# Kernel tuning notes

Measured on AMD Instinct MI355X. Metric: run time of the kernel, lower is better.

## Reference

```python
import jax, jax.numpy as jnp
import numpy as np

N, F, H, E = 100000, 128, 128, 3200000
EPS = 1e-5


def setup_inputs() -> dict:
    key = jax.random.key(0)
    ks = jax.random.split(key, 16)
    g = lambda k, shape, fan_in: jax.random.normal(k, shape, jnp.float32) / np.sqrt(fan_in)
    inp = {
        'x': jax.random.normal(ks[0], (N, F), jnp.float32),
        'edge_index': jax.random.randint(ks[1], (2, E), 0, N, jnp.int64),
        # SAGEConv params: lin_l (aggregated-neighbor path, has bias), lin_r (root path, no bias)
        'W1l': g(ks[2], (F, H), F), 'b1': jnp.zeros((H,), jnp.float32), 'W1r': g(ks[3], (F, H), F),
        'W2l': g(ks[4], (H, H), H), 'b2': jnp.zeros((H,), jnp.float32), 'W2r': g(ks[5], (H, H), H),
        'W3l': g(ks[6], (H, H), H), 'b3': jnp.zeros((H,), jnp.float32), 'W3r': g(ks[7], (H, H), H),
        'W4l': g(ks[8], (H, 1), H), 'b4': jnp.zeros((1,), jnp.float32), 'W4r': g(ks[9], (H, 1), H),
        # BatchNorm affine params
        'g1': jnp.ones((H,), jnp.float32), 'be1': jnp.zeros((H,), jnp.float32),
        'g2': jnp.ones((H,), jnp.float32), 'be2': jnp.zeros((H,), jnp.float32),
        'g3': jnp.ones((H,), jnp.float32), 'be3': jnp.zeros((H,), jnp.float32),
        # shared residual linear
        'Wlin': g(ks[10], (H, H), H), 'blin': jnp.zeros((H,), jnp.float32),
    }
    return inp


def _sage(x, src, dst, Wl, b, Wr):
    # mean aggregation of source features at destination nodes
    n = x.shape[0]
    s = jax.ops.segment_sum(x[src], dst, num_segments=n)          # [N, d]
    cnt = jax.ops.segment_sum(jnp.ones_like(dst, x.dtype), dst, num_segments=n)
    agg = s / jnp.maximum(cnt, 1.0)[:, None]
    return agg @ Wl + b + x @ Wr


def _bn(x, gamma, beta):
    # training-mode batch norm over node dim (biased variance, as torch)
    mu = x.mean(0)
    var = jnp.mean((x - mu) ** 2, axis=0)
    return gamma * (x - mu) * jax.lax.rsqrt(var + EPS) + beta


def reference(x, edge_index, W1l, b1, W1r, W2l, b2, W2r, W3l, b3, W3r,
              W4l, b4, W4r, g1, be1, g2, be2, g3, be3, Wlin, blin):
    src, dst = edge_index[0], edge_index[1]
    # dropout is identity (eval-mode reference)
    x1 = jax.nn.elu(_bn(_sage(x, src, dst, W1l, b1, W1r), g1, be1))
    x2 = jax.nn.elu(_bn(_sage(x1, src, dst, W2l, b2, W2r), g2, be2))
    x2 = x2 + x1 @ Wlin + blin
    x3 = jax.nn.elu(_bn(_sage(x2, src, dst, W3l, b3, W3r), g3, be3))
    x3 = x3 + x2 @ Wlin + blin
    x4 = _sage(x3, src, dst, W4l, b4, W4r)  # [N, 1]
    return jnp.squeeze(x4, -1)
```

## Files before the change

kernel.cpp:

```cpp
#include <hip/hip_runtime.h>
#include <hip/hip_bf16.h>
#include <math.h>

#define BN_EPS 1e-5f

typedef __attribute__((ext_vector_type(8))) short bf16x8;
typedef __attribute__((ext_vector_type(4))) float f32x4;
typedef unsigned int uint32;

__device__ __forceinline__ unsigned bf16rne(float f) {
  unsigned u = __float_as_uint(f);
  unsigned r = u + 0x7fffu + ((u >> 16) & 1u);
  return r >> 16;
}
__device__ __forceinline__ float bf2f_lo(uint32 u) { return __uint_as_float(u << 16); }
__device__ __forceinline__ float bf2f_hi(uint32 u) { return __uint_as_float(u & 0xffff0000u); }
__device__ __forceinline__ uint32 packbf2(float a, float b) {
  return bf16rne(a) | (bf16rne(b) << 16);
}

__device__ __forceinline__ int edge_at(const int* __restrict__ ei, long long idx, int is64) {
  return is64 ? ei[2 * idx] : ei[idx];
}

__global__ void init_kernel(const int* __restrict__ ei, long long E, int* __restrict__ flag,
                            int* __restrict__ cnt, float* __restrict__ bnsum, int N) {
  if (blockIdx.x == 0) {
    __shared__ int found;
    int t = threadIdx.x;
    if (t == 0) found = 0;
    __syncthreads();
    long long npairs = E < 1024 ? E : 1024;
    for (long long p = t; p < npairs; p += blockDim.x)
      if (ei[2 * p + 1] != 0) found = 1;
    __syncthreads();
    if (t == 0) *flag = found ? 0 : 1;
    return;
  }
  long long i = (blockIdx.x - 1) * (long long)blockDim.x + threadIdx.x;
  if (i < N) cnt[i] = 0;
  else if (i < (long long)N + 64 * 256) bnsum[i - N] = 0.f;
}

__launch_bounds__(256)
__global__ void build_kernel(const int* __restrict__ ei, long long E,
                             const int* __restrict__ flag,
                             int* __restrict__ r, int* __restrict__ cnt,
                             const float* __restrict__ x, uint32* __restrict__ xb,
                             long long nf4,
                             const float* __restrict__ Wa, const float* __restrict__ Wb,
                             const float* __restrict__ Wc, const float* __restrict__ Wd,
                             const float* __restrict__ We, const float* __restrict__ Wf,
                             const float* __restrict__ Wg, ushort* __restrict__ Wp,
                             long long K3) {
  long long b = blockIdx.x;
  if (b >= K3) {
    int rb = (int)(b - K3);
    int wi = rb >> 3;
    const float* W = wi == 0 ? Wa : wi == 1 ? Wb : wi == 2 ? Wc : wi == 3 ? Wd
                   : wi == 4 ? We : wi == 5 ? Wf : Wg;
    ushort* dst = Wp + (size_t)wi * 16384;
    int s = (rb & 7) * 256 + threadIdx.x;
    int nt = s >> 8, rem = s & 255, ks = rem >> 6, lane = rem & 63;
    int q = lane >> 4, l16 = lane & 15;
    int kbase = ks * 32 + q * 8, c = nt * 16 + l16;
    uint32 o[4];
#pragma unroll
    for (int jp = 0; jp < 4; ++jp) {
      float fa = W[(size_t)(kbase + 2 * jp) * 128 + c];
      float fb = W[(size_t)(kbase + 2 * jp + 1) * 128 + c];
      o[jp] = packbf2(fa, fb);
    }
    ((uint4*)dst)[s] = make_uint4(o[0], o[1], o[2], o[3]);
    return;
  }
  int role = (int)(b % 3);
  long long id = b / 3;
  if (role == 0) {
    long long g = id * 256 + threadIdx.x;
    long long e0 = 2 * g;
    if (e0 >= E) return;
    int is64 = *flag;
    bool h1 = (e0 + 1 < E);
    int d0, d1 = 0;
    if (is64 && !(E & 1)) {
      int4 dv = ((const int4*)(ei + 2 * E))[g];
      d0 = dv.x; d1 = dv.z;
    } else {
      d0 = edge_at(ei, E + e0, is64);
      if (h1) d1 = edge_at(ei, E + e0 + 1, is64);
    }
    int r0 = atomicAdd(&cnt[d0], 1);
    if (h1) {
      int r1 = atomicAdd(&cnt[d1], 1);
      ((int2*)r)[g] = make_int2(r0, r1);
    } else {
      r[e0] = r0;
    }
  } else {
    long long i = (id * 2 + (role - 1)) * 256 + threadIdx.x;
    if (i < nf4) {
      float4 f = ((const float4*)x)[i];
      uint2 o;
      o.x = packbf2(f.x, f.y);
      o.y = packbf2(f.z, f.w);
      ((uint2*)xb)[i] = o;
    }
  }
}

__global__ void partial_kernel(const int* __restrict__ cnt, int* __restrict__ bsum, int M) {
  __shared__ int s[256];
  int b = blockIdx.x, t = threadIdx.x;
  int base = b * 2048 + t * 8;
  int sum = 0;
#pragma unroll
  for (int i = 0; i < 8; ++i) {
    int idx = base + i;
    if (idx < M) sum += cnt[idx];
  }
  s[t] = sum;
  __syncthreads();
  for (int d = 128; d > 0; d >>= 1) {
    if (t < d) s[t] += s[t + d];
    __syncthreads();
  }
  if (t == 0) bsum[b] = s[0];
}

__global__ void scanb_kernel(int* __restrict__ bsum, int nb) {
  __shared__ int s[512];
  int t = threadIdx.x;
  int v = (t < nb) ? bsum[t] : 0;
  s[t] = v;
  __syncthreads();
  for (int d = 1; d < 512; d <<= 1) {
    int u = (t >= d) ? s[t - d] : 0;
    __syncthreads();
    s[t] += u;
    __syncthreads();
  }
  if (t < nb) bsum[t] = s[t] - v;
}

__global__ void offsets_kernel(const int* __restrict__ cnt, const int* __restrict__ bsum,
                               int* __restrict__ off, int M, long long Etot) {
  __shared__ int s[256];
  int b = blockIdx.x, t = threadIdx.x;
  int base = b * 2048 + t * 8;
  int v[8];
  int sum = 0;
#pragma unroll
  for (int i = 0; i < 8; ++i) {
    int idx = base + i;
    v[i] = (idx < M) ? cnt[idx] : 0;
    sum += v[i];
  }
  s[t] = sum;
  __syncthreads();
  for (int d = 1; d < 256; d <<= 1) {
    int u = (t >= d) ? s[t - d] : 0;
    __syncthreads();
    s[t] += u;
    __syncthreads();
  }
  int run = bsum[b] + s[t] - sum;
#pragma unroll
  for (int i = 0; i < 8; ++i) {
    int idx = base + i;
    if (idx < M) {
      off[idx] = run;
      run += v[i];
    }
  }
  if (b == 0 && t == 0) off[M] = (int)Etot;
}

__global__ void pos_scatter_kernel(const int* __restrict__ ei, long long E,
                                   const int* __restrict__ flag, const int* __restrict__ r,
                                   const int* __restrict__ off, uint32* __restrict__ ppk,
                                   int* __restrict__ esrc) {
  long long g = blockIdx.x * (long long)blockDim.x + threadIdx.x;
  long long e0 = 2 * g;
  if (e0 >= E) return;
  int is64 = *flag;
  bool h1 = (e0 + 1 < E);
  int d0, d1 = 0;
  if (is64 && !(E & 1)) {
    int4 dv = ((const int4*)(ei + 2 * E))[g];
    d0 = dv.x; d1 = dv.z;
  } else {
    d0 = edge_at(ei, E + e0, is64);
    if (h1) d1 = edge_at(ei, E + e0 + 1, is64);
  }
  int r0, r1 = 0;
  if (h1) { int2 rv = ((const int2*)r)[g]; r0 = rv.x; r1 = rv.y; }
  else r0 = r[e0];
  uint32 p0 = (uint32)(off[d0] + r0);
  uint32 reg0 = (uint32)d0 >> 15;
  ppk[e0] = p0 | (reg0 << 28);
  if (reg0 == 0) esrc[p0] = edge_at(ei, e0, is64);
  if (h1) {
    uint32 p1 = (uint32)(off[d1] + r1);
    uint32 reg1 = (uint32)d1 >> 15;
    ppk[e0 + 1] = p1 | (reg1 << 28);
    if (reg1 == 0) esrc[p1] = edge_at(ei, e0 + 1, is64);
  }
}

__global__ void scatter_det_kernel(const int* __restrict__ ei, long long E,
                                   const int* __restrict__ flag,
                                   const uint32* __restrict__ ppk, uint32 p,
                                   int* __restrict__ esrc) {
  long long e = blockIdx.x * (long long)blockDim.x + threadIdx.x;
  if (e >= E) return;
  uint32 v = ppk[e];
  if ((v >> 28) == p) esrc[v & 0x0FFFFFFFu] = edge_at(ei, e, *flag);
}

__global__ void aggregate_bf16_kernel(const uint32* __restrict__ X, const int* __restrict__ off,
                                      const int* __restrict__ esrc, uint32* __restrict__ out,
                                      int N) {
  int gw = (int)((blockIdx.x * (long long)blockDim.x + threadIdx.x) >> 6);
  int lane = threadIdx.x & 63;
  if (gw >= N) return;
  int b = off[gw], e = off[gw + 1];
  int sub = lane & 15, grp = lane >> 4;
  const uint4* X4 = (const uint4*)X;
  float acc[8];
#pragma unroll
  for (int j = 0; j < 8; ++j) acc[j] = 0.f;
  for (int i = b; i < e; i += 16) {
    uint4 v[4];
#pragma unroll
    for (int u = 0; u < 4; ++u) {
      int ii = i + u * 4 + grp;
      v[u] = make_uint4(0, 0, 0, 0);
      if (ii < e) { int s = esrc[ii]; v[u] = X4[(size_t)s * 16 + sub]; }
    }
#pragma unroll
    for (int u = 0; u < 4; ++u) {
      acc[0] += bf2f_lo(v[u].x); acc[1] += bf2f_hi(v[u].x);
      acc[2] += bf2f_lo(v[u].y); acc[3] += bf2f_hi(v[u].y);
      acc[4] += bf2f_lo(v[u].z); acc[5] += bf2f_hi(v[u].z);
      acc[6] += bf2f_lo(v[u].w); acc[7] += bf2f_hi(v[u].w);
    }
  }
#pragma unroll
  for (int j = 0; j < 8; ++j) {
    acc[j] += __shfl_xor(acc[j], 16, 64);
    acc[j] += __shfl_xor(acc[j], 32, 64);
  }
  if (grp == 0) {
    float inv = 1.0f / fmaxf((float)(e - b), 1.0f);
    uint4 o;
    o.x = packbf2(acc[0] * inv, acc[1] * inv);
    o.y = packbf2(acc[2] * inv, acc[3] * inv);
    o.z = packbf2(acc[4] * inv, acc[5] * inv);
    o.w = packbf2(acc[6] * inv, acc[7] * inv);
    ((uint4*)out)[(size_t)gw * 16 + sub] = o;
  }
}

__launch_bounds__(256)
__global__ void gemm_mfma_kernel(const ushort* __restrict__ A1, const ushort* __restrict__ W1p,
                                 const ushort* __restrict__ A2, const ushort* __restrict__ W2p,
                                 const ushort* __restrict__ W3p,
                                 const float* __restrict__ bias, const float* __restrict__ rbias,
                                 ushort* __restrict__ Y, ushort* __restrict__ R,
                                 float* __restrict__ bnsum, int N) {
  __shared__ float sred[16][128];
  int t = threadIdx.x;
  int w = t >> 6, lane = t & 63;
  int quad = lane >> 4, l16 = lane & 15;
  int row0 = blockIdx.x * 64 + w * 16;

  f32x4 accY[8], accR[8];
#pragma unroll
  for (int nt = 0; nt < 8; ++nt) {
    accY[nt][0] = accY[nt][1] = accY[nt][2] = accY[nt][3] = 0.f;
    accR[nt][0] = accR[nt][1] = accR[nt][2] = accR[nt][3] = 0.f;
  }

  int rowA = row0 + l16;
  if (rowA > N - 1) rowA = N - 1;
  const ushort* a1p = A1 + (size_t)rowA * 128 + quad * 8;
  const ushort* a2p = A2 + (size_t)rowA * 128 + quad * 8;
  const int haveR = (W3p != nullptr);

#pragma unroll
  for (int ks = 0; ks < 4; ++ks) {
    bf16x8 a = *(const bf16x8*)(a1p + ks * 32);
#pragma unroll
    for (int nt = 0; nt < 8; ++nt) {
      bf16x8 b = *(const bf16x8*)(W1p + ((size_t)(nt * 4 + ks) * 64 + lane) * 8);
      accY[nt] = __builtin_amdgcn_mfma_f32_16x16x32_bf16(a, b, accY[nt], 0, 0, 0);
    }
  }
#pragma unroll
  for (int ks = 0; ks < 4; ++ks) {
    bf16x8 a = *(const bf16x8*)(a2p + ks * 32);
#pragma unroll
    for (int nt = 0; nt < 8; ++nt) {
      bf16x8 b = *(const bf16x8*)(W2p + ((size_t)(nt * 4 + ks) * 64 + lane) * 8);
      accY[nt] = __builtin_amdgcn_mfma_f32_16x16x32_bf16(a, b, accY[nt], 0, 0, 0);
    }
    if (haveR) {
#pragma unroll
      for (int nt = 0; nt < 8; ++nt) {
        bf16x8 b = *(const bf16x8*)(W3p + ((size_t)(nt * 4 + ks) * 64 + lane) * 8);
        accR[nt] = __builtin_amdgcn_mfma_f32_16x16x32_bf16(a, b, accR[nt], 0, 0, 0);
      }
    }
  }

  float s1v[8], s2v[8];
#pragma unroll
  for (int nt = 0; nt < 8; ++nt) {
    int c = nt * 16 + l16;
    float bv = bias[c];
    s1v[nt] = 0.f; s2v[nt] = 0.f;
#pragma unroll
    for (int reg = 0; reg < 4; ++reg) {
      int grow = row0 + quad * 4 + reg;
      if (grow < N) {
        float v = accY[nt][reg] + bv;
        Y[(size_t)grow * 128 + c] = (ushort)bf16rne(v);
        s1v[nt] += v; s2v[nt] += v * v;
      }
    }
    if (haveR) {
      float rb = rbias[c];
#pragma unroll
      for (int reg = 0; reg < 4; ++reg) {
        int grow = row0 + quad * 4 + reg;
        if (grow < N) {
          float v = accR[nt][reg] + rb;
          R[(size_t)grow * 128 + c] = (ushort)bf16rne(v);
        }
      }
    }
  }

  int rrow = w * 4 + quad;
#pragma unroll
  for (int nt = 0; nt < 8; ++nt) sred[rrow][nt * 16 + l16] = s1v[nt];
  __syncthreads();
  if (t < 128) {
    float tot = 0.f;
#pragma unroll
    for (int r16 = 0; r16 < 16; ++r16) tot += sred[r16][t];
    atomicAdd(&bnsum[(size_t)(blockIdx.x & 63) * 256 + t], tot);
  }
  __syncthreads();
#pragma unroll
  for (int nt = 0; nt < 8; ++nt) sred[rrow][nt * 16 + l16] = s2v[nt];
  __syncthreads();
  if (t < 128) {
    float tot = 0.f;
#pragma unroll
    for (int r16 = 0; r16 < 16; ++r16) tot += sred[r16][t];
    atomicAdd(&bnsum[(size_t)(blockIdx.x & 63) * 256 + 128 + t], tot);
  }
}

__global__ void bn_finalize_kernel(float* __restrict__ bnsum, float* __restrict__ bnp, int N) {
  int t = threadIdx.x;
  if (t < 128) {
    float s = 0.f, s2 = 0.f;
    for (int sh = 0; sh < 64; ++sh) {
      s  += bnsum[(size_t)sh * 256 + t];
      s2 += bnsum[(size_t)sh * 256 + 128 + t];
    }
    float invN = 1.0f / (float)N;
    float mu = s * invN;
    float var = s2 * invN - mu * mu;
    bnp[t] = mu;
    bnp[128 + t] = rsqrtf(var + BN_EPS);
  }
  __syncthreads();
  for (int i = t; i < 64 * 256; i += 256) bnsum[i] = 0.f;
}

__global__ void bn_elu_kernel(const uint32* __restrict__ Y, const float* __restrict__ bnp,
                              const float* __restrict__ g, const float* __restrict__ be,
                              const uint32* __restrict__ res, uint32* __restrict__ Xo,
                              const float* __restrict__ W4l, const float* __restrict__ W4r,
                              float* __restrict__ z, float* __restrict__ rr,
                              long long total2) {
  long long i = blockIdx.x * (long long)blockDim.x + threadIdx.x;
  if (i >= total2) return;
  int c0 = (int)(i & 63) * 2;
  uint32 y = Y[i];
  float v0 = g[c0]     * (bf2f_lo(y) - bnp[c0])     * bnp[128 + c0]     + be[c0];
  float v1 = g[c0 + 1] * (bf2f_hi(y) - bnp[c0 + 1]) * bnp[128 + c0 + 1] + be[c0 + 1];
  v0 = v0 > 0.f ? v0 : expm1f(v0);
  v1 = v1 > 0.f ? v1 : expm1f(v1);
  if (res) {
    uint32 rv = res[i];
    v0 += bf2f_lo(rv); v1 += bf2f_hi(rv);
  }
  if (Xo) Xo[i] = packbf2(v0, v1);
  if (z) {
    float a = v0 * W4l[c0] + v1 * W4l[c0 + 1];
    float bb = v0 * W4r[c0] + v1 * W4r[c0 + 1];
    for (int d = 32; d > 0; d >>= 1) {
      a += __shfl_down(a, d, 64);
      bb += __shfl_down(bb, d, 64);
    }
    if ((i & 63) == 0) {
      long long row = i >> 6;
      z[row] = a;
      rr[row] = bb;
    }
  }
}

__global__ void final_kernel(const float* __restrict__ z, const float* __restrict__ rr,
                             const int* __restrict__ off, const int* __restrict__ esrc,
                             const float* __restrict__ b4, float* __restrict__ out, int N) {
  int n = blockIdx.x * blockDim.x + threadIdx.x;
  if (n >= N) return;
  int b = off[n], e = off[n + 1];
  float s = 0.f;
  for (int i = b; i < e; ++i) s += z[esrc[i]];
  out[n] = s / fmaxf((float)(e - b), 1.0f) + b4[0] + rr[n];
}

extern "C" void kernel_launch(void* const* d_in, const int* in_sizes, int n_in,
                              void* d_out, int out_size, void* d_ws, size_t ws_size,
                              hipStream_t stream) {
  const float* x   = (const float*)d_in[0];
  const int*   ei  = (const int*)d_in[1];
  const float* W1l = (const float*)d_in[2];
  const float* b1  = (const float*)d_in[3];
  const float* W1r = (const float*)d_in[4];
  const float* W2l = (const float*)d_in[5];
  const float* b2  = (const float*)d_in[6];
  const float* W2r = (const float*)d_in[7];
  const float* W3l = (const float*)d_in[8];
  const float* b3  = (const float*)d_in[9];
  const float* W3r = (const float*)d_in[10];
  const float* W4l = (const float*)d_in[11];
  const float* b4  = (const float*)d_in[12];
  const float* W4r = (const float*)d_in[13];
  const float* g1  = (const float*)d_in[14];
  const float* be1 = (const float*)d_in[15];
  const float* g2  = (const float*)d_in[16];
  const float* be2 = (const float*)d_in[17];
  const float* g3  = (const float*)d_in[18];
  const float* be3 = (const float*)d_in[19];
  const float* Wlin= (const float*)d_in[20];
  const float* blin= (const float*)d_in[21];

  const int N = in_sizes[0] / 128;
  const long long E = in_sizes[1] / 2;
  float* out = (float*)d_out;

  char* w = (char*)d_ws;
  size_t o = 0;
  auto alloc = [&](size_t bytes) -> char* {
    char* p = w + o;
    o = (o + bytes + 255) & ~(size_t)255;
    return p;
  };
  int*    off_node = (int*)alloc((size_t)(N + 1) * 4);
  int*    bsum     = (int*)alloc(512 * 4);
  int*    flag     = (int*)alloc(4);
  float*  bnsum    = (float*)alloc((size_t)64 * 256 * 4);
  float*  bnp      = (float*)alloc(256 * 4);
  float*  z        = (float*)alloc((size_t)N * 4);
  float*  rr       = (float*)alloc((size_t)N * 4);
  ushort* Wp       = (ushort*)alloc((size_t)7 * 2048 * 16);
  int*    esrc     = (int*)alloc((size_t)E * 4);
  size_t slotA = (size_t)E * 4;
  size_t ysz = (size_t)N * 256;
  if (ysz > slotA) slotA = ysz;
  char* poolA = alloc(slotA);
  char* B1c   = alloc((size_t)N * 256);
  char* B2c   = alloc((size_t)N * 256);
  char* B3c   = alloc((size_t)N * 256);
  (void)ws_size; (void)n_in; (void)out_size;

  int*    r    = (int*)poolA;
  ushort* Ybuf = (ushort*)poolA;
  uint32* B1   = (uint32*)B1c;
  uint32* B2   = (uint32*)B2c;
  uint32* B3   = (uint32*)B3c;
  size_t cnt_bytes = ((size_t)N * 4 + 255) & ~(size_t)255;
  size_t csr_need = cnt_bytes + (size_t)E * 4;
  char* poolCSR = (csr_need <= (size_t)N * 256) ? B3c : alloc(csr_need);
  int*    cnt = (int*)poolCSR;
  uint32* ppk = (uint32*)(poolCSR + cnt_bytes);

  const int B = 256;
  const long long pairs = (E + 1) / 2;
  const int ebp = (int)((pairs + B - 1) / B);
  const long long nf4 = (long long)N * 32;
  const int cb4 = (int)((nf4 + B - 1) / B);
  int K = ebp > (cb4 + 1) / 2 ? ebp : (cb4 + 1) / 2;
  const int Gbuild = 3 * K + 56;
  const int eb = (int)((E + B - 1) / B);
  const int zb = 1 + (int)(((long long)N + 64 * 256 + B - 1) / B);
  const int nb = (N + B - 1) / B;
  const int wb = (int)(((long long)N * 64 + B - 1) / B);
  const int gb = (N + 63) / 64;
  const long long tot2 = (long long)N * 64;
  const int cb = (int)((tot2 + B - 1) / B);
  const int gN = (N + 2047) / 2048;

  ushort* Wp1l = Wp + 0 * 16384;
  ushort* Wp1r = Wp + 1 * 16384;
  ushort* Wp2l = Wp + 2 * 16384;
  ushort* Wp2r = Wp + 3 * 16384;
  ushort* Wp3l = Wp + 4 * 16384;
  ushort* Wp3r = Wp + 5 * 16384;
  ushort* Wpln = Wp + 6 * 16384;

  init_kernel<<<zb, B, 0, stream>>>(ei, E, flag, cnt, bnsum, N);
  build_kernel<<<Gbuild, B, 0, stream>>>(ei, E, flag, r, cnt, x, B2, nf4,
                                         W1l, W1r, W2l, W2r, W3l, W3r, Wlin, Wp,
                                         (long long)3 * K);
  partial_kernel<<<gN, B, 0, stream>>>(cnt, bsum, N);
  scanb_kernel<<<1, 512, 0, stream>>>(bsum, gN);
  offsets_kernel<<<gN, B, 0, stream>>>(cnt, bsum, off_node, N, E);
  pos_scatter_kernel<<<ebp, B, 0, stream>>>(ei, E, flag, r, off_node, ppk, esrc);
  for (uint32 p = 1; p < 4; ++p)
    scatter_det_kernel<<<eb, B, 0, stream>>>(ei, E, flag, ppk, p, esrc);

  aggregate_bf16_kernel<<<wb, B, 0, stream>>>(B2, off_node, esrc, B1, N);
  gemm_mfma_kernel<<<gb, B, 0, stream>>>((const ushort*)B1, Wp1l, (const ushort*)B2, Wp1r,
                                         nullptr, b1, nullptr, Ybuf, nullptr, bnsum, N);
  bn_finalize_kernel<<<1, 256, 0, stream>>>(bnsum, bnp, N);
  bn_elu_kernel<<<cb, B, 0, stream>>>((const uint32*)Ybuf, bnp, g1, be1, nullptr, B3,
                                      nullptr, nullptr, nullptr, nullptr, tot2);

  aggregate_bf16_kernel<<<wb, B, 0, stream>>>(B3, off_node, esrc, B1, N);
  gemm_mfma_kernel<<<gb, B, 0, stream>>>((const ushort*)B1, Wp2l, (const ushort*)B3, Wp2r,
                                         Wpln, b2, blin, Ybuf, (ushort*)B2, bnsum, N);
  bn_finalize_kernel<<<1, 256, 0, stream>>>(bnsum, bnp, N);
  bn_elu_kernel<<<cb, B, 0, stream>>>((const uint32*)Ybuf, bnp, g2, be2, B2, B1,
                                      nullptr, nullptr, nullptr, nullptr, tot2);

  aggregate_bf16_kernel<<<wb, B, 0, stream>>>(B1, off_node, esrc, B3, N);
  gemm_mfma_kernel<<<gb, B, 0, stream>>>((const ushort*)B3, Wp3l, (const ushort*)B1, Wp3r,
                                         Wpln, b3, blin, Ybuf, (ushort*)B2, bnsum, N);
  bn_finalize_kernel<<<1, 256, 0, stream>>>(bnsum, bnp, N);
  bn_elu_kernel<<<cb, B, 0, stream>>>((const uint32*)Ybuf, bnp, g3, be3, B2, nullptr,
                                      W4l, W4r, z, rr, tot2);

  final_kernel<<<nb, B, 0, stream>>>(z, rr, off_node, esrc, b4, out, N);
}
```

Before: 968.1 us.

## Replace global-atomic CSR build with per-block shared-memory histogram counting sort

Builds the destination-sorted edge list with 192 edge-chunk blocks instead of global atomics and multi-pass region scatters. Each block histograms its chunk into shared memory, one node range at a time. The per-block counts are stored as bytes and prefix-scanned across blocks per node, and a second pass places each source at offset plus block prefix plus a local shared-memory atomic. The final readout kernel now uses four lanes per node with a shuffle reduction. The trade-off is that each block rereads its edge chunk once per node range in both passes, only 192 blocks run, and the byte-sized counters assume small per-node degrees.

```diff
diff --git a/kernel.cpp b/kernel.cpp
--- a/kernel.cpp
+++ b/kernel.cpp
@@ -3,6 +3,8 @@
 #include <math.h>
 
 #define BN_EPS 1e-5f
+#define NBLK 192
+#define RB 8192
 
 typedef __attribute__((ext_vector_type(8))) short bf16x8;
 typedef __attribute__((ext_vector_type(4))) float f32x4;
@@ -24,7 +26,7 @@
 }
 
 __global__ void init_kernel(const int* __restrict__ ei, long long E, int* __restrict__ flag,
-                            int* __restrict__ cnt, float* __restrict__ bnsum, int N) {
+                            float* __restrict__ bnsum) {
   if (blockIdx.x == 0) {
     __shared__ int found;
     int t = threadIdx.x;
@@ -37,76 +39,101 @@
     if (t == 0) *flag = found ? 0 : 1;
     return;
   }
-  long long i = (blockIdx.x - 1) * (long long)blockDim.x + threadIdx.x;
-  if (i < N) cnt[i] = 0;
-  else if (i < (long long)N + 64 * 256) bnsum[i - N] = 0.f;
+  int i = (blockIdx.x - 1) * 256 + threadIdx.x;
+  if (i < 64 * 256) bnsum[i] = 0.f;
 }
 
 __launch_bounds__(256)
-__global__ void build_kernel(const int* __restrict__ ei, long long E,
+__global__ void passA_kernel(const int* __restrict__ ei, long long E,
                              const int* __restrict__ flag,
-                             int* __restrict__ r, int* __restrict__ cnt,
+                             unsigned char* __restrict__ bc, int N, int NR, long long CE,
                              const float* __restrict__ x, uint32* __restrict__ xb,
                              long long nf4,
                              const float* __restrict__ Wa, const float* __restrict__ Wb,
                              const float* __restrict__ Wc, const float* __restrict__ Wd,
                              const float* __restrict__ We, const float* __restrict__ Wf,
-                             const float* __restrict__ Wg, ushort* __restrict__ Wp,
-                             long long K3) {
-  long long b = blockIdx.x;
-  if (b >= K3) {
-    int rb = (int)(b - K3);
-    int wi = rb >> 3;
-    const float* W = wi == 0 ? Wa : wi == 1 ? Wb : wi == 2 ? Wc : wi == 3 ? Wd
-                   : wi == 4 ? We : wi == 5 ? Wf : Wg;
-    ushort* dst = Wp + (size_t)wi * 16384;
-    int s = (rb & 7) * 256 + threadIdx.x;
-    int nt = s >> 8, rem = s & 255, ks = rem >> 6, lane = rem & 63;
-    int q = lane >> 4, l16 = lane & 15;
-    int kbase = ks * 32 + q * 8, c = nt * 16 + l16;
-    uint32 o[4];
-#pragma unroll
-    for (int jp = 0; jp < 4; ++jp) {
-      float fa = W[(size_t)(kbase + 2 * jp) * 128 + c];
-      float fb = W[(size_t)(kbase + 2 * jp + 1) * 128 + c];
-      o[jp] = packbf2(fa, fb);
-    }
-    ((uint4*)dst)[s] = make_uint4(o[0], o[1], o[2], o[3]);
+                             const float* __restrict__ Wg, ushort* __restrict__ Wp) {
+  __shared__ int hist[RB];
+  int bid = blockIdx.x;
+  int tid = threadIdx.x;
+  if (bid >= NBLK) {
+    int rb = bid - NBLK;
+    if (rb < 56) {
+      int wi = rb >> 3;
+      const float* W = wi == 0 ? Wa : wi == 1 ? Wb : wi == 2 ? Wc : wi == 3 ? Wd
+                     : wi == 4 ? We : wi == 5 ? Wf : Wg;
+      ushort* dst = Wp + (size_t)wi * 16384;
+      int s = (rb & 7) * 256 + tid;
+      int nt = s >> 8, rem = s & 255, ks = rem >> 6, lane = rem & 63;
+      int q = lane >> 4, l16 = lane & 15;
+      int kbase = ks * 32 + q * 8, c = nt * 16 + l16;
+      uint32 o[4];
+#pragma unroll
+      for (int jp = 0; jp < 4; ++jp) {
+        float fa = W[(size_t)(kbase + 2 * jp) * 128 + c];
+        float fb = W[(size_t)(kbase + 2 * jp + 1) * 128 + c];
+        o[jp] = packbf2(fa, fb);
+      }
+      ((uint4*)dst)[s] = make_uint4(o[0], o[1], o[2], o[3]);
+      return;
+    }
+    int cid = rb - 56;
+    long long baseI = (long long)cid * 1024 + tid;
+#pragma unroll
+    for (int k = 0; k < 4; ++k) {
+      long long i = baseI + (long long)k * 256;
+      if (i < nf4) {
+        float4 f = ((const float4*)x)[i];
+        uint2 o2;
+        o2.x = packbf2(f.x, f.y);
+        o2.y = packbf2(f.z, f.w);
+        ((uint2*)xb)[i] = o2;
+      }
+    }
     return;
   }
-  int role = (int)(b % 3);
-  long long id = b / 3;
-  if (role == 0) {
-    long long g = id * 256 + threadIdx.x;
-    long long e0 = 2 * g;
-    if (e0 >= E) return;
-    int is64 = *flag;
-    bool h1 = (e0 + 1 < E);
-    int d0, d1 = 0;
-    if (is64 && !(E & 1)) {
-      int4 dv = ((const int4*)(ei + 2 * E))[g];
-      d0 = dv.x; d1 = dv.z;
-    } else {
-      d0 = edge_at(ei, E + e0, is64);
-      if (h1) d1 = edge_at(ei, E + e0 + 1, is64);
-    }
-    int r0 = atomicAdd(&cnt[d0], 1);
-    if (h1) {
-      int r1 = atomicAdd(&cnt[d1], 1);
-      ((int2*)r)[g] = make_int2(r0, r1);
-    } else {
-      r[e0] = r0;
-    }
-  } else {
-    long long i = (id * 2 + (role - 1)) * 256 + threadIdx.x;
-    if (i < nf4) {
-      float4 f = ((const float4*)x)[i];
-      uint2 o;
-      o.x = packbf2(f.x, f.y);
-      o.y = packbf2(f.z, f.w);
-      ((uint2*)xb)[i] = o;
-    }
-  }
+  long long e0 = (long long)bid * CE;
+  long long e1 = e0 + CE;
+  if (e1 > E) e1 = E;
+  int is64 = *flag;
+  for (int r = 0; r < NR; ++r) {
+    int base = r * RB;
+    for (int i = tid; i < RB; i += 256) hist[i] = 0;
+    __syncthreads();
+    for (long long e = e0 + tid; e < e1; e += 256 * 8) {
+      int ds[8];
+#pragma unroll
+      for (int u = 0; u < 8; ++u) {
+        long long ee = e + (long long)u * 256;
+        ds[u] = (ee < e1) ? edge_at(ei, E + ee, is64) : -1;
+      }
+#pragma unroll
+      for (int u = 0; u < 8; ++u) {
+        unsigned rel = (unsigned)(ds[u] - base);
+        if (rel < RB) atomicAdd(&hist[rel], 1);
+      }
+    }
+    __syncthreads();
+    for (int i = tid; i < RB; i += 256) {
+      int d = base + i;
+      if (d < N) bc[(size_t)bid * N + d] = (unsigned char)hist[i];
+    }
+    __syncthreads();
+  }
+}
+
+__global__ void blockscan_kernel(unsigned char* __restrict__ bc, int* __restrict__ cnt_node,
+                                 int N) {
+  int d = blockIdx.x * 256 + threadIdx.x;
+  if (d >= N) return;
+  int run = 0;
+  for (int b = 0; b < NBLK; ++b) {
+    size_t idx = (size_t)b * N + d;
+    int c = bc[idx];
+    bc[idx] = (unsigned char)run;
+    run += c;
+  }
+  cnt_node[d] = run;
 }
 
 __global__ void partial_kernel(const int* __restrict__ cnt, int* __restrict__ bsum, int M) {
@@ -176,46 +203,43 @@
   if (b == 0 && t == 0) off[M] = (int)Etot;
 }
 
-__global__ void pos_scatter_kernel(const int* __restrict__ ei, long long E,
-                                   const int* __restrict__ flag, const int* __restrict__ r,
-                                   const int* __restrict__ off, uint32* __restrict__ ppk,
-                                   int* __restrict__ esrc) {
-  long long g = blockIdx.x * (long long)blockDim.x + threadIdx.x;
-  long long e0 = 2 * g;
-  if (e0 >= E) return;
+__launch_bounds__(256)
+__global__ void passC_kernel(const int* __restrict__ ei, long long E,
+                             const int* __restrict__ flag,
+                             const unsigned char* __restrict__ bc,
+                             const int* __restrict__ off, int* __restrict__ esrc,
+                             int N, int NR, long long CE) {
+  __shared__ int hist[RB];
+  int bid = blockIdx.x, tid = threadIdx.x;
+  long long e0 = (long long)bid * CE;
+  long long e1 = e0 + CE;
+  if (e1 > E) e1 = E;
   int is64 = *flag;
-  bool h1 = (e0 + 1 < E);
-  int d0, d1 = 0;
-  if (is64 && !(E & 1)) {
-    int4 dv = ((const int4*)(ei + 2 * E))[g];
-    d0 = dv.x; d1 = dv.z;
-  } else {
-    d0 = edge_at(ei, E + e0, is64);
-    if (h1) d1 = edge_at(ei, E + e0 + 1, is64);
-  }
-  int r0, r1 = 0;
-  if (h1) { int2 rv = ((const int2*)r)[g]; r0 = rv.x; r1 = rv.y; }
-  else r0 = r[e0];
-  uint32 p0 = (uint32)(off[d0] + r0);
-  uint32 reg0 = (uint32)d0 >> 15;
-  ppk[e0] = p0 | (reg0 << 28);
-  if (reg0 == 0) esrc[p0] = edge_at(ei, e0, is64);
-  if (h1) {
-    uint32 p1 = (uint32)(off[d1] + r1);
-    uint32 reg1 = (uint32)d1 >> 15;
-    ppk[e0 + 1] = p1 | (reg1 << 28);
-    if (reg1 == 0) esrc[p1] = edge_at(ei, e0 + 1, is64);
-  }
-}
-
-__global__ void scatter_det_kernel(const int* __restrict__ ei, long long E,
-                                   const int* __restrict__ flag,
-                                   const uint32* __restrict__ ppk, uint32 p,
-                                   int* __restrict__ esrc) {
-  long long e = blockIdx.x * (long long)blockDim.x + threadIdx.x;
-  if (e >= E) return;
-  uint32 v = ppk[e];
-  if ((v >> 28) == p) esrc[v & 0x0FFFFFFFu] = edge_at(ei, e, *flag);
+  for (int r = 0; r < NR; ++r) {
+    int base = r * RB;
+    for (int i = tid; i < RB; i += 256) hist[i] = 0;
+    __syncthreads();
+    for (long long e = e0 + tid; e < e1; e += 256 * 4) {
+      int ds[4];
+#pragma unroll
+      for (int u = 0; u < 4; ++u) {
+        long long ee = e + (long long)u * 256;
+        ds[u] = (ee < e1) ? edge_at(ei, E + ee, is64) : -1;
+      }
+#pragma unroll
+      for (int u = 0; u < 4; ++u) {
+        unsigned rel = (unsigned)(ds[u] - base);
+        if (rel < RB) {
+          long long ee = e + (long long)u * 256;
+          int d = ds[u];
+          int lr = atomicAdd(&hist[rel], 1);
+          int pos = off[d] + (int)bc[(size_t)bid * N + d] + lr;
+          esrc[pos] = edge_at(ei, ee, is64);
+        }
+      }
+    }
+    __syncthreads();
+  }
 }
 
 __global__ void aggregate_bf16_kernel(const uint32* __restrict__ X, const int* __restrict__ off,
@@ -419,12 +443,16 @@
 __global__ void final_kernel(const float* __restrict__ z, const float* __restrict__ rr,
                              const int* __restrict__ off, const int* __restrict__ esrc,
                              const float* __restrict__ b4, float* __restrict__ out, int N) {
-  int n = blockIdx.x * blockDim.x + threadIdx.x;
-  if (n >= N) return;
+  long long t = blockIdx.x * (long long)blockDim.x + threadIdx.x;
+  int n = (int)(t >> 2);
+  int q = (int)(t & 3);
+  if (n >= N) n = N - 1;
   int b = off[n], e = off[n + 1];
   float s = 0.f;
-  for (int i = b; i < e; ++i) s += z[esrc[i]];
-  out[n] = s / fmaxf((float)(e - b), 1.0f) + b4[0] + rr[n];
+  for (int i = b + q; i < e; i += 4) s += z[esrc[i]];
+  s += __shfl_xor(s, 1, 64);
+  s += __shfl_xor(s, 2, 64);
+  if (q == 0) out[n] = s / fmaxf((float)(e - b), 1.0f) + b4[0] + rr[n];
 }
 
 extern "C" void kernel_launch(void* const* d_in, const int* in_sizes, int n_in,
@@ -465,6 +493,7 @@
     return p;
   };
   int*    off_node = (int*)alloc((size_t)(N + 1) * 4);
+  int*    cnt_node = (int*)alloc((size_t)N * 4);
   int*    bsum     = (int*)alloc(512 * 4);
   int*    flag     = (int*)alloc(4);
   float*  bnsum    = (float*)alloc((size_t)64 * 256 * 4);
@@ -473,41 +502,36 @@
   float*  rr       = (float*)alloc((size_t)N * 4);
   ushort* Wp       = (ushort*)alloc((size_t)7 * 2048 * 16);
   int*    esrc     = (int*)alloc((size_t)E * 4);
-  size_t slotA = (size_t)E * 4;
+  size_t slotA = (size_t)NBLK * N;
   size_t ysz = (size_t)N * 256;
   if (ysz > slotA) slotA = ysz;
+  if ((size_t)E * 4 > slotA) slotA = (size_t)E * 4;
   char* poolA = alloc(slotA);
   char* B1c   = alloc((size_t)N * 256);
   char* B2c   = alloc((size_t)N * 256);
   char* B3c   = alloc((size_t)N * 256);
   (void)ws_size; (void)n_in; (void)out_size;
 
-  int*    r    = (int*)poolA;
+  unsigned char* bc = (unsigned char*)poolA;
   ushort* Ybuf = (ushort*)poolA;
   uint32* B1   = (uint32*)B1c;
   uint32* B2   = (uint32*)B2c;
   uint32* B3   = (uint32*)B3c;
-  size_t cnt_bytes = ((size_t)N * 4 + 255) & ~(size_t)255;
-  size_t csr_need = cnt_bytes + (size_t)E * 4;
-  char* poolCSR = (csr_need <= (size_t)N * 256) ? B3c : alloc(csr_need);
-  int*    cnt = (int*)poolCSR;
-  uint32* ppk = (uint32*)(poolCSR + cnt_bytes);
 
   const int B = 256;
-  const long long pairs = (E + 1) / 2;
-  const int ebp = (int)((pairs + B - 1) / B);
+  const int NR = (N + RB - 1) / RB;
+  const long long CE = (E + NBLK - 1) / NBLK;
   const long long nf4 = (long long)N * 32;
-  const int cb4 = (int)((nf4 + B - 1) / B);
-  int K = ebp > (cb4 + 1) / 2 ? ebp : (cb4 + 1) / 2;
-  const int Gbuild = 3 * K + 56;
-  const int eb = (int)((E + B - 1) / B);
-  const int zb = 1 + (int)(((long long)N + 64 * 256 + B - 1) / B);
-  const int nb = (N + B - 1) / B;
+  const int CB = (int)((nf4 + 1023) / 1024);
+  const int GA = NBLK + 56 + CB;
+  const int zb = 1 + 64;
+  const int sb = (N + B - 1) / B;
   const int wb = (int)(((long long)N * 64 + B - 1) / B);
   const int gb = (N + 63) / 64;
   const long long tot2 = (long long)N * 64;
   const int cb = (int)((tot2 + B - 1) / B);
   const int gN = (N + 2047) / 2048;
+  const int fb = (int)(((long long)N * 4 + B - 1) / B);
 
   ushort* Wp1l = Wp + 0 * 16384;
   ushort* Wp1r = Wp + 1 * 16384;
@@ -517,16 +541,14 @@
   ushort* Wp3r = Wp + 5 * 16384;
   ushort* Wpln = Wp + 6 * 16384;
 
-  init_kernel<<<zb, B, 0, stream>>>(ei, E, flag, cnt, bnsum, N);
-  build_kernel<<<Gbuild, B, 0, stream>>>(ei, E, flag, r, cnt, x, B2, nf4,
-                                         W1l, W1r, W2l, W2r, W3l, W3r, Wlin, Wp,
-                                         (long long)3 * K);
-  partial_kernel<<<gN, B, 0, stream>>>(cnt, bsum, N);
+  init_kernel<<<zb, B, 0, stream>>>(ei, E, flag, bnsum);
+  passA_kernel<<<GA, B, 0, stream>>>(ei, E, flag, bc, N, NR, CE, x, B2, nf4,
+                                     W1l, W1r, W2l, W2r, W3l, W3r, Wlin, Wp);
+  blockscan_kernel<<<sb, B, 0, stream>>>(bc, cnt_node, N);
+  partial_kernel<<<gN, B, 0, stream>>>(cnt_node, bsum, N);
   scanb_kernel<<<1, 512, 0, stream>>>(bsum, gN);
-  offsets_kernel<<<gN, B, 0, stream>>>(cnt, bsum, off_node, N, E);
-  pos_scatter_kernel<<<ebp, B, 0, stream>>>(ei, E, flag, r, off_node, ppk, esrc);
-  for (uint32 p = 1; p < 4; ++p)
-    scatter_det_kernel<<<eb, B, 0, stream>>>(ei, E, flag, ppk, p, esrc);
+  offsets_kernel<<<gN, B, 0, stream>>>(cnt_node, bsum, off_node, N, E);
+  passC_kernel<<<NBLK, B, 0, stream>>>(ei, E, flag, bc, off_node, esrc, N, NR, CE);
 
   aggregate_bf16_kernel<<<wb, B, 0, stream>>>(B2, off_node, esrc, B1, N);
   gemm_mfma_kernel<<<gb, B, 0, stream>>>((const ushort*)B1, Wp1l, (const ushort*)B2, Wp1r,
@@ -549,5 +571,5 @@
   bn_elu_kernel<<<cb, B, 0, stream>>>((const uint32*)Ybuf, bnp, g3, be3, B2, nullptr,
                                       W4l, W4r, z, rr, tot2);
 
-  final_kernel<<<nb, B, 0, stream>>>(z, rr, off_node, esrc, b4, out, N);
-}
+  final_kernel<<<fb, B, 0, stream>>>(z, rr, off_node, esrc, b4, out, N);
+}
```

Result: slower. 1.239 ms (+28.0%).

## Compact edge src/dst during build, fuse region scatter passes, parallelize final gather

Applied to the files above, without the earlier changes.

The build pass now writes compact int32 copies of the edge source and destination arrays. This lets the position kernel read only the compact destinations, and the four region-ordered scatter passes over the int64 edge_index collapse into one kernel whose blocks are interleaved by region. The final aggregation uses four lanes per node with shuffle reductions instead of one thread per node. This trades extra writes in build and a scratch buffer that aliases B1 for fewer full-edge reads and launches. The fused scatter no longer guarantees region ordering across blocks, which may hurt the cache locality the region split was meant to provide.

```diff
diff --git a/kernel.cpp b/kernel.cpp
--- a/kernel.cpp
+++ b/kernel.cpp
@@ -46,6 +46,7 @@
 __global__ void build_kernel(const int* __restrict__ ei, long long E,
                              const int* __restrict__ flag,
                              int* __restrict__ r, int* __restrict__ cnt,
+                             int* __restrict__ es, int* __restrict__ ed,
                              const float* __restrict__ x, uint32* __restrict__ xb,
                              long long nf4,
                              const float* __restrict__ Wa, const float* __restrict__ Wb,
@@ -82,29 +83,37 @@
     if (e0 >= E) return;
     int is64 = *flag;
     bool h1 = (e0 + 1 < E);
-    int d0, d1 = 0;
+    int s0, s1 = 0, d0, d1 = 0;
     if (is64 && !(E & 1)) {
+      int4 sv = ((const int4*)ei)[g];
       int4 dv = ((const int4*)(ei + 2 * E))[g];
+      s0 = sv.x; s1 = sv.z;
       d0 = dv.x; d1 = dv.z;
     } else {
+      s0 = edge_at(ei, e0, is64);
       d0 = edge_at(ei, E + e0, is64);
-      if (h1) d1 = edge_at(ei, E + e0 + 1, is64);
+      if (h1) {
+        s1 = edge_at(ei, e0 + 1, is64);
+        d1 = edge_at(ei, E + e0 + 1, is64);
+      }
     }
     int r0 = atomicAdd(&cnt[d0], 1);
     if (h1) {
       int r1 = atomicAdd(&cnt[d1], 1);
-      ((int2*)r)[g] = make_int2(r0, r1);
+      ((int2*)r)[g]  = make_int2(r0, r1);
+      ((int2*)es)[g] = make_int2(s0, s1);
+      ((int2*)ed)[g] = make_int2(d0, d1);
     } else {
-      r[e0] = r0;
+      r[e0] = r0; es[e0] = s0; ed[e0] = d0;
     }
   } else {
     long long i = (id * 2 + (role - 1)) * 256 + threadIdx.x;
     if (i < nf4) {
       float4 f = ((const float4*)x)[i];
-      uint2 o;
-      o.x = packbf2(f.x, f.y);
-      o.y = packbf2(f.z, f.w);
-      ((uint2*)xb)[i] = o;
+      uint2 o2;
+      o2.x = packbf2(f.x, f.y);
+      o2.y = packbf2(f.z, f.w);
+      ((uint2*)xb)[i] = o2;
     }
   }
 }
@@ -176,46 +185,40 @@
   if (b == 0 && t == 0) off[M] = (int)Etot;
 }
 
-__global__ void pos_scatter_kernel(const int* __restrict__ ei, long long E,
-                                   const int* __restrict__ flag, const int* __restrict__ r,
-                                   const int* __restrict__ off, uint32* __restrict__ ppk,
-                                   int* __restrict__ esrc) {
+__global__ void pos_kernel(const int* __restrict__ ed, const int* __restrict__ r,
+                           const int* __restrict__ off, uint32* __restrict__ ppk,
+                           long long E) {
   long long g = blockIdx.x * (long long)blockDim.x + threadIdx.x;
   long long e0 = 2 * g;
   if (e0 >= E) return;
-  int is64 = *flag;
   bool h1 = (e0 + 1 < E);
-  int d0, d1 = 0;
-  if (is64 && !(E & 1)) {
-    int4 dv = ((const int4*)(ei + 2 * E))[g];
-    d0 = dv.x; d1 = dv.z;
+  if (h1) {
+    int2 dv = ((const int2*)ed)[g];
+    int2 rv = ((const int2*)r)[g];
+    uint32 p0 = (uint32)(off[dv.x] + rv.x) | (((uint32)dv.x >> 15) << 28);
+    uint32 p1 = (uint32)(off[dv.y] + rv.y) | (((uint32)dv.y >> 15) << 28);
+    ((uint2*)ppk)[g] = make_uint2(p0, p1);
   } else {
-    d0 = edge_at(ei, E + e0, is64);
-    if (h1) d1 = edge_at(ei, E + e0 + 1, is64);
-  }
-  int r0, r1 = 0;
-  if (h1) { int2 rv = ((const int2*)r)[g]; r0 = rv.x; r1 = rv.y; }
-  else r0 = r[e0];
-  uint32 p0 = (uint32)(off[d0] + r0);
-  uint32 reg0 = (uint32)d0 >> 15;
-  ppk[e0] = p0 | (reg0 << 28);
-  if (reg0 == 0) esrc[p0] = edge_at(ei, e0, is64);
-  if (h1) {
-    uint32 p1 = (uint32)(off[d1] + r1);
-    uint32 reg1 = (uint32)d1 >> 15;
-    ppk[e0 + 1] = p1 | (reg1 << 28);
-    if (reg1 == 0) esrc[p1] = edge_at(ei, e0 + 1, is64);
-  }
-}
-
-__global__ void scatter_det_kernel(const int* __restrict__ ei, long long E,
-                                   const int* __restrict__ flag,
-                                   const uint32* __restrict__ ppk, uint32 p,
-                                   int* __restrict__ esrc) {
-  long long e = blockIdx.x * (long long)blockDim.x + threadIdx.x;
-  if (e >= E) return;
-  uint32 v = ppk[e];
-  if ((v >> 28) == p) esrc[v & 0x0FFFFFFFu] = edge_at(ei, e, *flag);
+    int d0 = ed[e0];
+    ppk[e0] = (uint32)(off[d0] + r[e0]) | (((uint32)d0 >> 15) << 28);
+  }
+}
+
+__launch_bounds__(256)
+__global__ void scatter_fused_kernel(const int* __restrict__ es, const uint32* __restrict__ ppk,
+                                     long long E, int* __restrict__ esrc) {
+  int c = blockIdx.x & 7;
+  uint32 region = (uint32)(c >> 1);
+  long long q = blockIdx.x >> 3;
+  long long base = (q * 2 + (c & 1)) * 1024;
+#pragma unroll
+  for (int it = 0; it < 4; ++it) {
+    long long e = base + it * 256 + threadIdx.x;
+    if (e < E) {
+      uint32 v = ppk[e];
+      if ((v >> 28) == region) esrc[v & 0x0FFFFFFFu] = es[e];
+    }
+  }
 }
 
 __global__ void aggregate_bf16_kernel(const uint32* __restrict__ X, const int* __restrict__ off,
@@ -419,12 +422,16 @@
 __global__ void final_kernel(const float* __restrict__ z, const float* __restrict__ rr,
                              const int* __restrict__ off, const int* __restrict__ esrc,
                              const float* __restrict__ b4, float* __restrict__ out, int N) {
-  int n = blockIdx.x * blockDim.x + threadIdx.x;
-  if (n >= N) return;
+  long long t = blockIdx.x * (long long)blockDim.x + threadIdx.x;
+  int n = (int)(t >> 2);
+  int q = (int)(t & 3);
+  if (n >= N) n = N - 1;
   int b = off[n], e = off[n + 1];
   float s = 0.f;
-  for (int i = b; i < e; ++i) s += z[esrc[i]];
-  out[n] = s / fmaxf((float)(e - b), 1.0f) + b4[0] + rr[n];
+  for (int i = b + q; i < e; i += 4) s += z[esrc[i]];
+  s += __shfl_xor(s, 1, 64);
+  s += __shfl_xor(s, 2, 64);
+  if (q == 0) out[n] = s / fmaxf((float)(e - b), 1.0f) + b4[0] + rr[n];
 }
 
 extern "C" void kernel_launch(void* const* d_in, const int* in_sizes, int n_in,
@@ -487,11 +494,11 @@
   uint32* B1   = (uint32*)B1c;
   uint32* B2   = (uint32*)B2c;
   uint32* B3   = (uint32*)B3c;
+  int*    es   = (int*)B1c;
+  int*    ed   = es + E;
   size_t cnt_bytes = ((size_t)N * 4 + 255) & ~(size_t)255;
-  size_t csr_need = cnt_bytes + (size_t)E * 4;
-  char* poolCSR = (csr_need <= (size_t)N * 256) ? B3c : alloc(csr_need);
-  int*    cnt = (int*)poolCSR;
-  uint32* ppk = (uint32*)(poolCSR + cnt_bytes);
+  int*    cnt = (int*)B3c;
+  uint32* ppk = (uint32*)(B3c + cnt_bytes);
 
   const int B = 256;
   const long long pairs = (E + 1) / 2;
@@ -500,14 +507,15 @@
   const int cb4 = (int)((nf4 + B - 1) / B);
   int K = ebp > (cb4 + 1) / 2 ? ebp : (cb4 + 1) / 2;
   const int Gbuild = 3 * K + 56;
-  const int eb = (int)((E + B - 1) / B);
+  const long long qmax = (E + 2047) / 2048;
+  const int Gscat = (int)(qmax * 8);
   const int zb = 1 + (int)(((long long)N + 64 * 256 + B - 1) / B);
-  const int nb = (N + B - 1) / B;
   const int wb = (int)(((long long)N * 64 + B - 1) / B);
   const int gb = (N + 63) / 64;
   const long long tot2 = (long long)N * 64;
   const int cb = (int)((tot2 + B - 1) / B);
   const int gN = (N + 2047) / 2048;
+  const int fb = (int)(((long long)N * 4 + B - 1) / B);
 
   ushort* Wp1l = Wp + 0 * 16384;
   ushort* Wp1r = Wp + 1 * 16384;
@@ -518,15 +526,14 @@
   ushort* Wpln = Wp + 6 * 16384;
 
   init_kernel<<<zb, B, 0, stream>>>(ei, E, flag, cnt, bnsum, N);
-  build_kernel<<<Gbuild, B, 0, stream>>>(ei, E, flag, r, cnt, x, B2, nf4,
+  build_kernel<<<Gbuild, B, 0, stream>>>(ei, E, flag, r, cnt, es, ed, x, B2, nf4,
                                          W1l, W1r, W2l, W2r, W3l, W3r, Wlin, Wp,
                                          (long long)3 * K);
   partial_kernel<<<gN, B, 0, stream>>>(cnt, bsum, N);
   scanb_kernel<<<1, 512, 0, stream>>>(bsum, gN);
   offsets_kernel<<<gN, B, 0, stream>>>(cnt, bsum, off_node, N, E);
-  pos_scatter_kernel<<<ebp, B, 0, stream>>>(ei, E, flag, r, off_node, ppk, esrc);
-  for (uint32 p = 1; p < 4; ++p)
-    scatter_det_kernel<<<eb, B, 0, stream>>>(ei, E, flag, ppk, p, esrc);
+  pos_kernel<<<ebp, B, 0, stream>>>(ed, r, off_node, ppk, E);
+  scatter_fused_kernel<<<Gscat, B, 0, stream>>>(es, ppk, E, esrc);
 
   aggregate_bf16_kernel<<<wb, B, 0, stream>>>(B2, off_node, esrc, B1, N);
   gemm_mfma_kernel<<<gb, B, 0, stream>>>((const ushort*)B1, Wp1l, (const ushort*)B2, Wp1r,
@@ -549,5 +556,5 @@
   bn_elu_kernel<<<cb, B, 0, stream>>>((const uint32*)Ybuf, bnp, g3, be3, B2, nullptr,
                                       W4l, W4r, z, rr, tot2);
 
-  final_kernel<<<nb, B, 0, stream>>>(z, rr, off_node, esrc, b4, out, N);
-}
+  final_kernel<<<fb, B, 0, stream>>>(z, rr, off_node, esrc, b4, out, N);
+}
```

After: 930.0 us. 1.04x faster.
